# Optimization experiments

Hardware: AMD Instinct MI355X
Metric: run time of the kernel (lower is better)

The kernel has to match this reference:

```python
import jax, jax.numpy as jnp
import numpy as np

EMBED_DIM = 512
N_HEADS = 8
HEAD_DIM = EMBED_DIM // N_HEADS
MAX_H = 64
MAX_W = 48
B, H, W = 2, 64, 48


def setup_inputs() -> dict:
    key = jax.random.key(0)
    k1, k2, k3, k4, k5 = jax.random.split(key, 5)
    x = jax.random.normal(k1, (B, H, W, EMBED_DIM), dtype=jnp.float32)
    # Linear weights stored as [in, out] (torch stores [out, in]; math is x @ W_in_out)
    w_qkv = jax.random.normal(k2, (EMBED_DIM, 3 * EMBED_DIM), dtype=jnp.float32) * (EMBED_DIM ** -0.5)
    w_out = jax.random.normal(k3, (EMBED_DIM, EMBED_DIM), dtype=jnp.float32) * (EMBED_DIM ** -0.5)
    rel_row_tab = jax.random.normal(k4, (2 * MAX_H - 1, N_HEADS), dtype=jnp.float32) * 0.02
    rel_col_tab = jax.random.normal(k5, (2 * MAX_W - 1, N_HEADS), dtype=jnp.float32) * 0.02
    return {"x": x, "w_qkv": w_qkv, "w_out": w_out,
            "rel_row_tab": rel_row_tab, "rel_col_tab": rel_col_tab}


def _rel_bias(rel_row_tab, rel_col_tab, height, width):
    # 2D relative position bias: [n_heads, S, S]
    row_idx = jnp.repeat(jnp.arange(height), width)          # [S]
    col_idx = jnp.tile(jnp.arange(width), height)            # [S]
    rel_row = jnp.clip(row_idx[:, None] - row_idx[None, :] + MAX_H - 1, 0, 2 * MAX_H - 2)
    rel_col = jnp.clip(col_idx[:, None] - col_idx[None, :] + MAX_W - 1, 0, 2 * MAX_W - 2)
    bias = rel_row_tab[rel_row] + rel_col_tab[rel_col]       # [S, S, n_heads]
    return jnp.transpose(bias, (2, 0, 1))                    # [n_heads, S, S]


def reference(x, w_qkv, w_out, rel_row_tab, rel_col_tab):
    b, h, w, d = x.shape
    s = h * w
    x_flat = x.reshape(b, s, d)
    qkv = x_flat @ w_qkv                                     # [b, s, 3d]
    qkv = qkv.reshape(b, s, 3, N_HEADS, HEAD_DIM)
    qkv = jnp.transpose(qkv, (2, 0, 3, 1, 4))                # [3, b, nh, s, hd]
    q, k, v = qkv[0], qkv[1], qkv[2]
    scale = HEAD_DIM ** -0.5
    attn = jnp.einsum('bhqd,bhkd->bhqk', q, k) * scale       # [b, nh, s, s]
    attn = attn + _rel_bias(rel_row_tab, rel_col_tab, h, w)[None]
    attn = jax.nn.softmax(attn, axis=-1)
    out = jnp.einsum('bhqk,bhkd->bhqd', attn, v)             # [b, nh, s, hd]
    out = jnp.transpose(out, (0, 2, 1, 3)).reshape(b, s, d)
    out = out @ w_out
    return out.reshape(b, h, w, d)
```

## Files before the change

### kernel.cpp

```cpp
#include <hip/hip_runtime.h>
#include <hip/hip_bf16.h>

#define S_TOK 3072
#define NHEADS 8

typedef __attribute__((ext_vector_type(8))) short short8;
typedef __attribute__((ext_vector_type(4))) float floatx4;
typedef __attribute__((ext_vector_type(4))) unsigned short ushortx4;

__device__ __forceinline__ unsigned short f2bf(float f) {
  union { float f; unsigned u; } v; v.f = f;
  unsigned r = v.u + 0x7fffu + ((v.u >> 16) & 1u);
  return (unsigned short)(r >> 16);
}
__device__ __forceinline__ float bf2f(unsigned short h) {
  union { unsigned u; float f; } v; v.u = (unsigned)h << 16;
  return v.f;
}
__device__ __forceinline__ unsigned pack2bf(float a, float b) {
  __hip_bfloat162 h = __float22bfloat162_rn(make_float2(a, b));
  union { __hip_bfloat162 h; unsigned u; } c; c.h = h;
  return c.u;
}
__device__ __forceinline__ void gload16(const void* g, void* l) {
  __builtin_amdgcn_global_load_lds(
      (const __attribute__((address_space(1))) unsigned int*)g,
      (__attribute__((address_space(3))) unsigned int*)l, 16, 0, 0);
}

__global__ __launch_bounds__(256) void ga_conv_all(
    const float* __restrict__ X, const float* __restrict__ Wq,
    const float* __restrict__ Wo, unsigned short* __restrict__ xh,
    unsigned short* __restrict__ xl, unsigned short* __restrict__ wqh,
    unsigned short* __restrict__ wql, unsigned short* __restrict__ woh,
    unsigned short* __restrict__ wol) {
  const int blk = blockIdx.x;
  const int t = threadIdx.x;
  if (blk < 1536) {
    const int c = blk * 256 + t;
    const int m = c >> 6;
    const int c8 = (c & 63) << 3;
    const float* src = X + (size_t)m * 512 + c8;
    float4 v0 = *(const float4*)src, v1 = *(const float4*)(src + 4);
    float vv[8] = {v0.x, v0.y, v0.z, v0.w, v1.x, v1.y, v1.z, v1.w};
    union { unsigned short s[8]; short8 v; } hh, ll;
#pragma unroll
    for (int e = 0; e < 8; ++e) {
      hh.s[e] = f2bf(vv[e]);
      ll.s[e] = f2bf(vv[e] - bf2f(hh.s[e]));
    }
    const size_t dst = (size_t)m * 512 + (c8 ^ ((m & 7) << 3));
    *(short8*)&xh[dst] = hh.v;
    *(short8*)&xl[dst] = ll.v;
    return;
  }
  const int wq = (blk < 1728);
  const int b2 = wq ? (blk - 1536) : (blk - 1728);
  const int N = wq ? 1536 : 512;
  const float* W = wq ? Wq : Wo;
  unsigned short* th = wq ? wqh : woh;
  unsigned short* tl = wq ? wql : wol;
  const int k0 = (b2 & 7) * 64, n0 = (b2 >> 3) * 64;
  __shared__ float Ts[64][65];
#pragma unroll
  for (int i = 0; i < 4; ++i) {
    const int r = (t >> 4) + i * 16, c4 = (t & 15) * 4;
    float4 v = *(const float4*)&W[(size_t)(k0 + r) * N + n0 + c4];
    Ts[r][c4] = v.x; Ts[r][c4 + 1] = v.y; Ts[r][c4 + 2] = v.z; Ts[r][c4 + 3] = v.w;
  }
  __syncthreads();
#pragma unroll
  for (int j = 0; j < 2; ++j) {
    const int chunk = t * 2 + j;
    const int nl = chunk >> 3, m8 = chunk & 7;
    const int n = n0 + nl;
    const int ks = (m8 * 8) ^ ((n & 7) << 3);
    union { unsigned short s[8]; short8 v; } hh, ll;
#pragma unroll
    for (int e = 0; e < 8; ++e) {
      float f = Ts[ks + e][nl];
      hh.s[e] = f2bf(f);
      ll.s[e] = f2bf(f - bf2f(hh.s[e]));
    }
    const size_t dst = (size_t)n * 512 + k0 + m8 * 8;
    *(short8*)&th[dst] = hh.v;
    *(short8*)&tl[dst] = ll.v;
  }
}

template <int BM, int BN, int WHICH>
__global__ __launch_bounds__(256, 2) void ga_mm3(
    const unsigned short* __restrict__ Ah, const unsigned short* __restrict__ Al,
    const unsigned short* __restrict__ Bh, const unsigned short* __restrict__ Bl,
    unsigned short* __restrict__ Qd, unsigned short* __restrict__ Kd,
    unsigned short* __restrict__ Vd, float* __restrict__ Out) {
  const int tid = threadIdx.x;
  const int w = tid >> 6, l = tid & 63;
  const int g = l >> 4, ln = l & 15;
  const int wm = w >> 1, wn = w & 1;
  const int m0 = blockIdx.x * BM;
  const int n0 = blockIdx.y * BN;
  constexpr int MI = BM / 32;
  constexpr int NI = BN / 32;
  __shared__ unsigned short Alds[2][BM * 64];
  __shared__ unsigned short Blds[2][BN * 64];
  floatx4 acc[MI][NI];
#pragma unroll
  for (int mi = 0; mi < MI; ++mi)
#pragma unroll
    for (int ni = 0; ni < NI; ++ni)
#pragma unroll
      for (int r = 0; r < 4; ++r) acc[mi][ni][r] = 0.f;

  for (int k0 = 0; k0 < 512; k0 += 64) {
    __syncthreads();
    {
      constexpr int PWA = (BM * 128) / 4096;
      constexpr int PWB = (BN * 128) / 4096;
      const char* ga_h = (const char*)(Ah + (size_t)m0 * 512 + k0);
      const char* ga_l = (const char*)(Al + (size_t)m0 * 512 + k0);
      const char* gb_h = (const char*)(Bh + (size_t)n0 * 512 + k0);
      const char* gb_l = (const char*)(Bl + (size_t)n0 * 512 + k0);
#pragma unroll
      for (int i = 0; i < PWA; ++i) {
        const int off = (w * PWA + i) * 1024;
        const int gb = ((off >> 7) + (l >> 3)) * 1024 + (l & 7) * 16;
        gload16(ga_h + gb, (char*)&Alds[0][0] + off);
        gload16(ga_l + gb, (char*)&Alds[1][0] + off);
      }
#pragma unroll
      for (int i = 0; i < PWB; ++i) {
        const int off = (w * PWB + i) * 1024;
        const int gb = ((off >> 7) + (l >> 3)) * 1024 + (l & 7) * 16;
        gload16(gb_h + gb, (char*)&Blds[0][0] + off);
        gload16(gb_l + gb, (char*)&Blds[1][0] + off);
      }
    }
    asm volatile("s_waitcnt vmcnt(0)" ::: "memory");
    __syncthreads();
#pragma unroll
    for (int kk = 0; kk < 64; kk += 32) {
      const int kbase = kk + g * 8;
      short8 ah[MI], al[MI], bh[NI], bl[NI];
#pragma unroll
      for (int mi = 0; mi < MI; ++mi) {
        const int row = wm * (BM / 2) + mi * 16 + ln;
        const int a = row * 64 + (kbase ^ ((row & 7) << 3));
        ah[mi] = *(const short8*)&Alds[0][a];
        al[mi] = *(const short8*)&Alds[1][a];
      }
#pragma unroll
      for (int ni = 0; ni < NI; ++ni) {
        const int row = wn * (BN / 2) + ni * 16 + ln;
        const int a = row * 64 + (kbase ^ ((row & 7) << 3));
        bh[ni] = *(const short8*)&Blds[0][a];
        bl[ni] = *(const short8*)&Blds[1][a];
      }
#pragma unroll
      for (int mi = 0; mi < MI; ++mi)
#pragma unroll
        for (int ni = 0; ni < NI; ++ni) {
          acc[mi][ni] = __builtin_amdgcn_mfma_f32_16x16x32_bf16(
              ah[mi], bh[ni], acc[mi][ni], 0, 0, 0);
          acc[mi][ni] = __builtin_amdgcn_mfma_f32_16x16x32_bf16(
              al[mi], bh[ni], acc[mi][ni], 0, 0, 0);
          acc[mi][ni] = __builtin_amdgcn_mfma_f32_16x16x32_bf16(
              ah[mi], bl[ni], acc[mi][ni], 0, 0, 0);
        }
    }
  }
  if constexpr (WHICH == 0) {
    const int b = m0 / S_TOK;
    const int s_base = (m0 % S_TOK) + wm * (BM / 2);
#pragma unroll
    for (int ni = 0; ni < NI; ++ni) {
      const int ng = n0 + wn * (BN / 2) + ni * 16;
      const int which = ng >> 9;
      const int h = (ng >> 6) & 7;
      const int d = (ng & 63) + ln;
      unsigned short* hp = (which == 0 ? Qd : which == 1 ? Kd : Vd) +
                           (size_t)(b * 8 + h) * S_TOK * 64;
      const float qs = (which == 0) ? 0.18033688f : 1.0f;
#pragma unroll
      for (int mi = 0; mi < MI; ++mi)
#pragma unroll
        for (int r = 0; r < 4; ++r) {
          const int s = s_base + mi * 16 + g * 4 + r;
          const size_t idx =
              (size_t)s * 64 + ((which == 1) ? (d ^ ((s & 7) << 3)) : d);
          hp[idx] = f2bf(acc[mi][ni][r] * qs);
        }
    }
  } else {
#pragma unroll
    for (int mi = 0; mi < MI; ++mi)
#pragma unroll
      for (int ni = 0; ni < NI; ++ni)
#pragma unroll
        for (int r = 0; r < 4; ++r)
          Out[(size_t)(m0 + wm * (BM / 2) + mi * 16 + g * 4 + r) * 512 + n0 +
              wn * (BN / 2) + ni * 16 + ln] = acc[mi][ni][r];
  }
}

__global__ __launch_bounds__(256) void ga_vtrans(
    const unsigned short* __restrict__ V, unsigned short* __restrict__ Vt2) {
  const int t = threadIdx.x;
  const int tile = blockIdx.x;
  const int bh = blockIdx.y;
  __shared__ unsigned short Ts[96][72];
  const unsigned short* vp = V + ((size_t)bh * S_TOK + tile * 96) * 64;
#pragma unroll
  for (int it = 0; it < 3; ++it) {
    int c = it * 256 + t;
    int s = c >> 3, d8 = c & 7;
    short8 v = *(const short8*)&vp[(size_t)s * 64 + d8 * 8];
    *(short8*)&Ts[s][d8 * 8] = v;
  }
  __syncthreads();
  unsigned short* op = Vt2 + ((size_t)bh * 32 + tile) * 8192;
#pragma unroll
  for (int it = 0; it < 4; ++it) {
    int c2 = it * 256 + t;
    int a = c2 * 8;
    int d = a >> 7;
    int pos0 = (a & 127) ^ ((d & 7) << 3);
    short8 o;
    if (pos0 < 96) {
      const int base = (pos0 & 96) + ((pos0 >> 3) & 3) * 4;
#pragma unroll
      for (int j = 0; j < 8; ++j) {
        const int key = base + ((j >> 2) << 4) + (j & 3);
        o[j] = (short)Ts[key][d];
      }
    } else {
#pragma unroll
      for (int j = 0; j < 8; ++j) o[j] = 0;
    }
    *(short8*)&op[a] = o;
  }
}

__global__ __launch_bounds__(256) void ga_attn16(
    const unsigned short* __restrict__ Q, const unsigned short* __restrict__ Kg,
    const unsigned short* __restrict__ Vt2, const float* __restrict__ rowtab,
    const float* __restrict__ coltab, float* __restrict__ Opart,
    float* __restrict__ Lpart, int tiles_per_split) {
  const int tid = threadIdx.x;
  const int w = tid >> 6;
  const int l = tid & 63;
  const int g = l >> 4;
  const int ln = l & 15;
  const int bh = blockIdx.y;
  const int sp = blockIdx.z;
  const int h = bh & 7;
  const int q0 = blockIdx.x * 128 + w * 32;

  __shared__ float rtab[127];
  __shared__ float ctab[95];
  __shared__ unsigned short Klds[6144];
  __shared__ unsigned short Vlds[8192];
  for (int i = tid; i < 127; i += 256) rtab[i] = rowtab[i * 8 + h] * 1.44269504f;
  for (int i = tid; i < 95; i += 256) ctab[i] = coltab[i * 8 + h] * 1.44269504f;
  __syncthreads();

  const unsigned short* Qp = Q + (size_t)bh * S_TOK * 64;
  const unsigned short* Kp = Kg + (size_t)bh * S_TOK * 64;
  const unsigned short* Vp = Vt2 + (size_t)bh * 32 * 8192;

  int qr[2], qc[2];
  short8 qf[2][2];
  float ctr[2][3][4];
#pragma unroll
  for (int u = 0; u < 2; ++u) {
    const int q = q0 + u * 16 + ln;
    qr[u] = q / 48;
    qc[u] = q - qr[u] * 48;
    qf[u][0] = *(const short8*)&Qp[(size_t)q * 64 + g * 8];
    qf[u][1] = *(const short8*)&Qp[(size_t)q * 64 + 32 + g * 8];
    const float* cb = &ctab[qc[u] - g * 4 + 47];
#pragma unroll
    for (int m = 0; m < 3; ++m)
#pragma unroll
      for (int r = 0; r < 4; ++r) ctr[u][m][r] = cb[-(16 * m + r)];
  }

  short8 ones;
  {
    union { unsigned short s[8]; short8 v; } on;
#pragma unroll
    for (int j = 0; j < 8; ++j) on.s[j] = 0x3F80;
    ones = on.v;
  }

  floatx4 o_acc[2][4];
  floatx4 o5[2];
#pragma unroll
  for (int u = 0; u < 2; ++u) {
#pragma unroll
    for (int r = 0; r < 4; ++r) o5[u][r] = 0.f;
#pragma unroll
    for (int dt = 0; dt < 4; ++dt)
#pragma unroll
      for (int r = 0; r < 4; ++r) o_acc[u][dt][r] = 0.f;
  }

  const int t0 = sp * tiles_per_split;
  for (int t = t0; t < t0 + tiles_per_split; ++t) {
    __syncthreads();
    {
      const char* kg = (const char*)(Kp + (size_t)t * 96 * 64);
      const char* vg = (const char*)(Vp + (size_t)t * 8192);
#pragma unroll
      for (int i = 0; i < 3; ++i) {
        const int off = w * 3072 + i * 1024;
        gload16(kg + off + l * 16, (char*)Klds + off);
      }
#pragma unroll
      for (int i = 0; i < 4; ++i) {
        const int off = w * 4096 + i * 1024;
        gload16(vg + off + l * 16, (char*)Vlds + off);
      }
      asm volatile("s_waitcnt vmcnt(0)" ::: "memory");
      __syncthreads();
    }
    float rt[2][2];
#pragma unroll
    for (int u = 0; u < 2; ++u) {
      rt[u][0] = rtab[qr[u] + 63 - 2 * t] - 12.0f;
      rt[u][1] = rtab[qr[u] + 62 - 2 * t] - 12.0f;
    }
    const int swz = (ln & 7) << 3;
#pragma unroll
    for (int kc32 = 0; kc32 < 3; ++kc32) {
      float e[2][2][4];
#pragma unroll
      for (int kh = 0; kh < 2; ++kh) {
        const int kt = kc32 * 2 + kh;
        const int rb = (kt * 16 + ln) * 64;
        short8 kf0 = *(const short8*)&Klds[rb + ((g * 8) ^ swz)];
        short8 kf1 = *(const short8*)&Klds[rb + ((32 + g * 8) ^ swz)];
        const int m = kt % 3, wrap = kt / 3;
#pragma unroll
        for (int u = 0; u < 2; ++u) {
          floatx4 s = {0.f, 0.f, 0.f, 0.f};
          s = __builtin_amdgcn_mfma_f32_16x16x32_bf16(kf0, qf[u][0], s, 0, 0, 0);
          s = __builtin_amdgcn_mfma_f32_16x16x32_bf16(kf1, qf[u][1], s, 0, 0, 0);
          const float rtw = rt[u][wrap];
#pragma unroll
          for (int r = 0; r < 4; ++r)
            e[u][kh][r] = __builtin_amdgcn_exp2f(s[r] + rtw + ctr[u][m][r]);
        }
      }
      short8 pf[2];
#pragma unroll
      for (int u = 0; u < 2; ++u) {
        union { unsigned uu[4]; short8 v; } pk;
        pk.uu[0] = pack2bf(e[u][0][0], e[u][0][1]);
        pk.uu[1] = pack2bf(e[u][0][2], e[u][0][3]);
        pk.uu[2] = pack2bf(e[u][1][0], e[u][1][1]);
        pk.uu[3] = pack2bf(e[u][1][2], e[u][1][3]);
        pf[u] = pk.v;
      }
#pragma unroll
      for (int dt = 0; dt < 4; ++dt) {
        const int vrow = dt * 16 + ln;
        short8 vf = *(const short8*)&Vlds[vrow * 128 +
                                          ((kc32 * 32 + g * 8) ^ swz)];
        o_acc[0][dt] =
            __builtin_amdgcn_mfma_f32_16x16x32_bf16(pf[0], vf, o_acc[0][dt], 0, 0, 0);
        o_acc[1][dt] =
            __builtin_amdgcn_mfma_f32_16x16x32_bf16(pf[1], vf, o_acc[1][dt], 0, 0, 0);
      }
      o5[0] = __builtin_amdgcn_mfma_f32_16x16x32_bf16(pf[0], ones, o5[0], 0, 0, 0);
      o5[1] = __builtin_amdgcn_mfma_f32_16x16x32_bf16(pf[1], ones, o5[1], 0, 0, 0);
    }
  }
  const size_t rowbase = (size_t)(sp * 16 + bh) * S_TOK;
#pragma unroll
  for (int u = 0; u < 2; ++u) {
    if (ln == 0) {
#pragma unroll
      for (int r = 0; r < 4; ++r)
        Lpart[rowbase + q0 + u * 16 + g * 4 + r] = o5[u][r];
    }
#pragma unroll
    for (int dt = 0; dt < 4; ++dt)
#pragma unroll
      for (int r = 0; r < 4; ++r)
        Opart[(rowbase + q0 + u * 16 + g * 4 + r) * 64 + dt * 16 + ln] =
            o_acc[u][dt][r];
  }
}

template <int NS>
__global__ __launch_bounds__(256) void ga_combine(
    const float* __restrict__ Opart, const float* __restrict__ Lpart,
    unsigned short* __restrict__ ch, unsigned short* __restrict__ cl) {
  const int c = blockIdx.x * 256 + threadIdx.x;
  const int m = c >> 6;
  const int col8 = (c & 63) << 3;
  const int b = (m >= S_TOK) ? 1 : 0;
  const int q = m - b * S_TOK;
  const int h = col8 >> 6, d0 = col8 & 63;
  const int bh = b * 8 + h;
  float v[8] = {0.f, 0.f, 0.f, 0.f, 0.f, 0.f, 0.f, 0.f};
  float ls = 0.f;
#pragma unroll
  for (int s = 0; s < NS; ++s) {
    const size_t row = (size_t)(s * 16 + bh) * S_TOK + q;
    ls += Lpart[row];
    const float4 o0 = *(const float4*)&Opart[row * 64 + d0];
    const float4 o1 = *(const float4*)&Opart[row * 64 + d0 + 4];
    v[0] += o0.x; v[1] += o0.y; v[2] += o0.z; v[3] += o0.w;
    v[4] += o1.x; v[5] += o1.y; v[6] += o1.z; v[7] += o1.w;
  }
  const float inv = 1.0f / ls;
  union { unsigned short s[8]; short8 vv; } hh, ll;
#pragma unroll
  for (int e = 0; e < 8; ++e) {
    float f = v[e] * inv;
    hh.s[e] = f2bf(f);
    ll.s[e] = f2bf(f - bf2f(hh.s[e]));
  }
  const size_t dst = (size_t)m * 512 + (col8 ^ ((m & 7) << 3));
  *(short8*)&ch[dst] = hh.vv;
  *(short8*)&cl[dst] = ll.vv;
}

extern "C" void kernel_launch(void* const* d_in, const int* in_sizes, int n_in,
                              void* d_out, int out_size, void* d_ws,
                              size_t ws_size, hipStream_t stream) {
  const float* x = (const float*)d_in[0];
  const float* w_qkv = (const float*)d_in[1];
  const float* w_out = (const float*)d_in[2];
  const float* rrow = (const float*)d_in[3];
  const float* rcol = (const float*)d_in[4];
  float* out = (float*)d_out;

  unsigned short* ws16 = (unsigned short*)d_ws;
  unsigned short* xh = ws16;
  unsigned short* xl = xh + 3145728;
  unsigned short* wqh = xl + 3145728;
  unsigned short* wql = wqh + 786432;
  unsigned short* woh = wql + 786432;
  unsigned short* wol = woh + 262144;
  unsigned short* Qb = wol + 262144;
  unsigned short* Kb = Qb + 3145728;
  unsigned short* Vb = Kb + 3145728;
  unsigned short* Vt2 = Vb + 3145728;
  float* Opart = (float*)(Vt2 + 4194304);
  const size_t base_bytes = (size_t)22020096 * 2;
  const size_t per_split = (size_t)(3145728 + 49152) * 4;
  int nsplit = (ws_size >= base_bytes + 4 * per_split) ? 4
             : (ws_size >= base_bytes + 2 * per_split) ? 2 : 1;
  float* Lpart = Opart + (size_t)nsplit * 3145728;

  ga_conv_all<<<1792, 256, 0, stream>>>(x, w_qkv, w_out, xh, xl, wqh, wql, woh,
                                        wol);
  ga_mm3<128, 128, 0><<<dim3(48, 12), 256, 0, stream>>>(
      xh, xl, wqh, wql, Qb, Kb, Vb, nullptr);
  ga_vtrans<<<dim3(32, 16), 256, 0, stream>>>(Vb, Vt2);
  ga_attn16<<<dim3(24, 16, nsplit), 256, 0, stream>>>(
      Qb, Kb, Vt2, rrow, rcol, Opart, Lpart, 32 / nsplit);
  if (nsplit == 4)
    ga_combine<4><<<1536, 256, 0, stream>>>(Opart, Lpart, xh, xl);
  else if (nsplit == 2)
    ga_combine<2><<<1536, 256, 0, stream>>>(Opart, Lpart, xh, xl);
  else
    ga_combine<1><<<1536, 256, 0, stream>>>(Opart, Lpart, xh, xl);
  ga_mm3<64, 64, 1><<<dim3(96, 8), 256, 0, stream>>>(
      xh, xl, woh, wol, nullptr, nullptr, nullptr, out);
}
```

Baseline: 135.2 us.

## Fuse split-K combine into output projection and drop bf16 hi/lo split

Merges the split-attention combine kernel into the output projection GEMM. Each block now reduces the partial O and L values per head, normalizes them, packs them to bf16 in LDS and runs MFMAs against the high half of W_out directly. This removes one launch and the round trip of the combined activations through global memory, and cuts the output GEMM from three MFMAs per step to one by dropping the lo correction terms. It also caps the attention split at 2, which lowers partial-reduction traffic but reduces parallelism. The cost is lower precision on the output projection, and the partial reductions are recomputed by every N-block (8 times).

```diff
diff --git a/kernel.cpp b/kernel.cpp
--- a/kernel.cpp
+++ b/kernel.cpp
@@ -88,12 +88,12 @@
   }
 }
 
-template <int BM, int BN, int WHICH>
+template <int BM, int BN>
 __global__ __launch_bounds__(256, 2) void ga_mm3(
     const unsigned short* __restrict__ Ah, const unsigned short* __restrict__ Al,
     const unsigned short* __restrict__ Bh, const unsigned short* __restrict__ Bl,
     unsigned short* __restrict__ Qd, unsigned short* __restrict__ Kd,
-    unsigned short* __restrict__ Vd, float* __restrict__ Out) {
+    unsigned short* __restrict__ Vd) {
   const int tid = threadIdx.x;
   const int w = tid >> 6, l = tid & 63;
   const int g = l >> 4, ln = l & 15;
@@ -169,37 +169,26 @@
         }
     }
   }
-  if constexpr (WHICH == 0) {
-    const int b = m0 / S_TOK;
-    const int s_base = (m0 % S_TOK) + wm * (BM / 2);
-#pragma unroll
-    for (int ni = 0; ni < NI; ++ni) {
-      const int ng = n0 + wn * (BN / 2) + ni * 16;
-      const int which = ng >> 9;
-      const int h = (ng >> 6) & 7;
-      const int d = (ng & 63) + ln;
-      unsigned short* hp = (which == 0 ? Qd : which == 1 ? Kd : Vd) +
-                           (size_t)(b * 8 + h) * S_TOK * 64;
-      const float qs = (which == 0) ? 0.18033688f : 1.0f;
-#pragma unroll
-      for (int mi = 0; mi < MI; ++mi)
-#pragma unroll
-        for (int r = 0; r < 4; ++r) {
-          const int s = s_base + mi * 16 + g * 4 + r;
-          const size_t idx =
-              (size_t)s * 64 + ((which == 1) ? (d ^ ((s & 7) << 3)) : d);
-          hp[idx] = f2bf(acc[mi][ni][r] * qs);
-        }
-    }
-  } else {
+  const int b = m0 / S_TOK;
+  const int s_base = (m0 % S_TOK) + wm * (BM / 2);
+#pragma unroll
+  for (int ni = 0; ni < NI; ++ni) {
+    const int ng = n0 + wn * (BN / 2) + ni * 16;
+    const int which = ng >> 9;
+    const int h = (ng >> 6) & 7;
+    const int d = (ng & 63) + ln;
+    unsigned short* hp = (which == 0 ? Qd : which == 1 ? Kd : Vd) +
+                         (size_t)(b * 8 + h) * S_TOK * 64;
+    const float qs = (which == 0) ? 0.18033688f : 1.0f;
 #pragma unroll
     for (int mi = 0; mi < MI; ++mi)
 #pragma unroll
-      for (int ni = 0; ni < NI; ++ni)
-#pragma unroll
-        for (int r = 0; r < 4; ++r)
-          Out[(size_t)(m0 + wm * (BM / 2) + mi * 16 + g * 4 + r) * 512 + n0 +
-              wn * (BN / 2) + ni * 16 + ln] = acc[mi][ni][r];
+      for (int r = 0; r < 4; ++r) {
+        const int s = s_base + mi * 16 + g * 4 + r;
+        const size_t idx =
+            (size_t)s * 64 + ((which == 1) ? (d ^ ((s & 7) << 3)) : d);
+        hp[idx] = f2bf(acc[mi][ni][r] * qs);
+      }
   }
 }
 
@@ -394,38 +383,105 @@
 }
 
 template <int NS>
-__global__ __launch_bounds__(256) void ga_combine(
+__global__ __launch_bounds__(256, 2) void ga_outmm(
     const float* __restrict__ Opart, const float* __restrict__ Lpart,
-    unsigned short* __restrict__ ch, unsigned short* __restrict__ cl) {
-  const int c = blockIdx.x * 256 + threadIdx.x;
-  const int m = c >> 6;
-  const int col8 = (c & 63) << 3;
+    const unsigned short* __restrict__ Bh_, float* __restrict__ Out) {
+  const int tid = threadIdx.x;
+  const int w = tid >> 6, l = tid & 63;
+  const int g = l >> 4, ln = l & 15;
+  const int wm = w >> 1, wn = w & 1;
+  const int m0 = blockIdx.x * 64;
+  const int n0 = blockIdx.y * 64;
+  __shared__ unsigned short Alds[64 * 64];
+  __shared__ unsigned short Blds[64 * 64];
+  floatx4 acc[2][2];
+#pragma unroll
+  for (int mi = 0; mi < 2; ++mi)
+#pragma unroll
+    for (int ni = 0; ni < 2; ++ni)
+#pragma unroll
+      for (int r = 0; r < 4; ++r) acc[mi][ni][r] = 0.f;
+
+  const int lm = tid >> 2, lk4 = tid & 3;
+  const int m = m0 + lm;
   const int b = (m >= S_TOK) ? 1 : 0;
   const int q = m - b * S_TOK;
-  const int h = col8 >> 6, d0 = col8 & 63;
-  const int bh = b * 8 + h;
-  float v[8] = {0.f, 0.f, 0.f, 0.f, 0.f, 0.f, 0.f, 0.f};
-  float ls = 0.f;
-#pragma unroll
-  for (int s = 0; s < NS; ++s) {
-    const size_t row = (size_t)(s * 16 + bh) * S_TOK + q;
-    ls += Lpart[row];
-    const float4 o0 = *(const float4*)&Opart[row * 64 + d0];
-    const float4 o1 = *(const float4*)&Opart[row * 64 + d0 + 4];
-    v[0] += o0.x; v[1] += o0.y; v[2] += o0.z; v[3] += o0.w;
-    v[4] += o1.x; v[5] += o1.y; v[6] += o1.z; v[7] += o1.w;
-  }
-  const float inv = 1.0f / ls;
-  union { unsigned short s[8]; short8 vv; } hh, ll;
-#pragma unroll
-  for (int e = 0; e < 8; ++e) {
-    float f = v[e] * inv;
-    hh.s[e] = f2bf(f);
-    ll.s[e] = f2bf(f - bf2f(hh.s[e]));
-  }
-  const size_t dst = (size_t)m * 512 + (col8 ^ ((m & 7) << 3));
-  *(short8*)&ch[dst] = hh.vv;
-  *(short8*)&cl[dst] = ll.vv;
+
+  for (int h = 0; h < 8; ++h) {
+    __syncthreads();
+    {
+      const char* gb = (const char*)(Bh_ + (size_t)n0 * 512 + h * 64);
+#pragma unroll
+      for (int i = 0; i < 2; ++i) {
+        const int off = (w * 2 + i) * 1024;
+        const int gbo = ((off >> 7) + (l >> 3)) * 1024 + (l & 7) * 16;
+        gload16(gb + gbo, (char*)Blds + off);
+      }
+    }
+    {
+      const int bh = b * 8 + h;
+      float v[16];
+      float ls = 0.f;
+#pragma unroll
+      for (int s = 0; s < NS; ++s) {
+        const size_t row = (size_t)(s * 16 + bh) * S_TOK + q;
+        ls += Lpart[row];
+        const float* op = &Opart[row * 64 + lk4 * 16];
+#pragma unroll
+        for (int j = 0; j < 4; ++j) {
+          float4 o = *(const float4*)(op + j * 4);
+          if (s == 0) {
+            v[j * 4] = o.x; v[j * 4 + 1] = o.y;
+            v[j * 4 + 2] = o.z; v[j * 4 + 3] = o.w;
+          } else {
+            v[j * 4] += o.x; v[j * 4 + 1] += o.y;
+            v[j * 4 + 2] += o.z; v[j * 4 + 3] += o.w;
+          }
+        }
+      }
+      const float inv = 1.0f / ls;
+      unsigned pk[8];
+#pragma unroll
+      for (int j = 0; j < 8; ++j)
+        pk[j] = pack2bf(v[2 * j] * inv, v[2 * j + 1] * inv);
+      const int sw = (lm & 7) << 3;
+      unsigned short* ab = &Alds[lm * 64];
+#pragma unroll
+      for (int j = 0; j < 4; ++j)
+        *(uint2*)&ab[(lk4 * 16 + j * 4) ^ sw] = make_uint2(pk[2 * j], pk[2 * j + 1]);
+    }
+    asm volatile("s_waitcnt vmcnt(0)" ::: "memory");
+    __syncthreads();
+#pragma unroll
+    for (int kk = 0; kk < 64; kk += 32) {
+      const int kbase = kk + g * 8;
+      short8 af[2], bf[2];
+#pragma unroll
+      for (int mi = 0; mi < 2; ++mi) {
+        const int row = wm * 32 + mi * 16 + ln;
+        af[mi] = *(const short8*)&Alds[row * 64 + (kbase ^ ((row & 7) << 3))];
+      }
+#pragma unroll
+      for (int ni = 0; ni < 2; ++ni) {
+        const int row = wn * 32 + ni * 16 + ln;
+        bf[ni] = *(const short8*)&Blds[row * 64 + (kbase ^ ((row & 7) << 3))];
+      }
+#pragma unroll
+      for (int mi = 0; mi < 2; ++mi)
+#pragma unroll
+        for (int ni = 0; ni < 2; ++ni)
+          acc[mi][ni] = __builtin_amdgcn_mfma_f32_16x16x32_bf16(
+              af[mi], bf[ni], acc[mi][ni], 0, 0, 0);
+    }
+  }
+#pragma unroll
+  for (int mi = 0; mi < 2; ++mi)
+#pragma unroll
+    for (int ni = 0; ni < 2; ++ni)
+#pragma unroll
+      for (int r = 0; r < 4; ++r)
+        Out[(size_t)(m0 + wm * 32 + mi * 16 + g * 4 + r) * 512 + n0 +
+            wn * 32 + ni * 16 + ln] = acc[mi][ni][r];
 }
 
 extern "C" void kernel_launch(void* const* d_in, const int* in_sizes, int n_in,
@@ -452,23 +508,18 @@
   float* Opart = (float*)(Vt2 + 4194304);
   const size_t base_bytes = (size_t)22020096 * 2;
   const size_t per_split = (size_t)(3145728 + 49152) * 4;
-  int nsplit = (ws_size >= base_bytes + 4 * per_split) ? 4
-             : (ws_size >= base_bytes + 2 * per_split) ? 2 : 1;
+  const int nsplit = (ws_size >= base_bytes + 2 * per_split) ? 2 : 1;
   float* Lpart = Opart + (size_t)nsplit * 3145728;
 
   ga_conv_all<<<1792, 256, 0, stream>>>(x, w_qkv, w_out, xh, xl, wqh, wql, woh,
                                         wol);
-  ga_mm3<128, 128, 0><<<dim3(48, 12), 256, 0, stream>>>(
-      xh, xl, wqh, wql, Qb, Kb, Vb, nullptr);
+  ga_mm3<128, 128><<<dim3(48, 12), 256, 0, stream>>>(
+      xh, xl, wqh, wql, Qb, Kb, Vb);
   ga_vtrans<<<dim3(32, 16), 256, 0, stream>>>(Vb, Vt2);
   ga_attn16<<<dim3(24, 16, nsplit), 256, 0, stream>>>(
       Qb, Kb, Vt2, rrow, rcol, Opart, Lpart, 32 / nsplit);
-  if (nsplit == 4)
-    ga_combine<4><<<1536, 256, 0, stream>>>(Opart, Lpart, xh, xl);
-  else if (nsplit == 2)
-    ga_combine<2><<<1536, 256, 0, stream>>>(Opart, Lpart, xh, xl);
+  if (nsplit == 2)
+    ga_outmm<2><<<dim3(96, 8), 256, 0, stream>>>(Opart, Lpart, woh, out);
   else
-    ga_combine<1><<<1536, 256, 0, stream>>>(Opart, Lpart, xh, xl);
-  ga_mm3<64, 64, 1><<<dim3(96, 8), 256, 0, stream>>>(
-      xh, xl, woh, wol, nullptr, nullptr, nullptr, out);
-}
+    ga_outmm<1><<<dim3(96, 8), 256, 0, stream>>>(Opart, Lpart, woh, out);
+}
```

Result: faster. 131.1 us (-3.0%).
